# Performance work log

Measured on AMD Instinct MI355X. Metric: run time of the kernel, lower is better.

Reference implementation:

```python
import jax, jax.numpy as jnp
import numpy as np

N_NODES = 10000
N_EDGES = 320000
IN_DIM = 512
HID = 64
H0 = 8
OUT = 64
H1 = 1
NEG_SLOPE = 0.2


def gat_layer(h, src, dst, W, attn_l, attn_r, n_nodes, activation=None):
    # h: (N, F_in); W: (F_in, H*D); attn_l/attn_r: (H, D)
    H, D = attn_l.shape
    feat = (h @ W).reshape(n_nodes, H, D)            # (N, H, D)
    el = jnp.einsum('nhd,hd->nh', feat, attn_l)      # (N, H)
    er = jnp.einsum('nhd,hd->nh', feat, attn_r)      # (N, H)
    e = jax.nn.leaky_relu(el[src] + er[dst], NEG_SLOPE)  # (E, H)
    # edge softmax over incoming edges of each destination node
    m = jax.ops.segment_max(e, dst, num_segments=n_nodes)   # (N, H), -inf for isolated
    m = jnp.where(jnp.isfinite(m), m, 0.0)
    ex = jnp.exp(e - m[dst])                         # (E, H)
    s = jax.ops.segment_sum(ex, dst, num_segments=n_nodes)  # (N, H)
    alpha = ex / s[dst]                              # (E, H)
    # weighted aggregation: out[dst] += alpha * feat[src]
    out = jax.ops.segment_sum(alpha[:, :, None] * feat[src], dst,
                              num_segments=n_nodes)  # (N, H, D)
    if activation is not None:
        out = activation(out)
    return out


def setup_inputs() -> dict:
    key = jax.random.key(0)
    ks = jax.random.split(key, 9)
    h = jax.random.normal(ks[0], (N_NODES, IN_DIM), dtype=jnp.float32)
    src = jax.random.randint(ks[1], (N_EDGES,), 0, N_NODES, dtype=jnp.int32)
    dst = jax.random.randint(ks[2], (N_EDGES,), 0, N_NODES, dtype=jnp.int32)
    W1 = jax.random.normal(ks[3], (IN_DIM, H0 * HID), dtype=jnp.float32) / np.sqrt(IN_DIM)
    attn_l1 = jax.random.normal(ks[4], (H0, HID), dtype=jnp.float32) / np.sqrt(HID)
    attn_r1 = jax.random.normal(ks[5], (H0, HID), dtype=jnp.float32) / np.sqrt(HID)
    W2 = jax.random.normal(ks[6], (H0 * HID, H1 * OUT), dtype=jnp.float32) / np.sqrt(H0 * HID)
    attn_l2 = jax.random.normal(ks[7], (H1, OUT), dtype=jnp.float32) / np.sqrt(OUT)
    attn_r2 = jax.random.normal(ks[8], (H1, OUT), dtype=jnp.float32) / np.sqrt(OUT)
    return {"h": h, "src": src, "dst": dst, "W1": W1, "attn_l1": attn_l1,
            "attn_r1": attn_r1, "W2": W2, "attn_l2": attn_l2, "attn_r2": attn_r2}


def reference(h, src, dst, W1, attn_l1, attn_r1, W2, attn_l2, attn_r2):
    # layer 1: elu activation, concat heads (flatten)
    x = gat_layer(h, src, dst, W1, attn_l1, attn_r1, N_NODES, activation=jax.nn.elu)
    x = x.reshape(N_NODES, H0 * HID)
    # layer 2: no activation, mean over heads
    x = gat_layer(x, src, dst, W2, attn_l2, attn_r2, N_NODES, activation=None)
    return x.mean(axis=1)  # (N, OUT)
```

## Files before the change

### kernel.cpp

```cpp
#include <hip/hip_runtime.h>
#include <hip/hip_bf16.h>
#include <math.h>

typedef unsigned int u32;
typedef unsigned short ushort;

constexpr int N_NODES = 10000;
constexpr int N_EDGES = 320000;
constexpr float NEG_SLOPE = 0.2f;

typedef __attribute__((ext_vector_type(8))) short short8;
typedef __attribute__((ext_vector_type(4))) float f32x4;
typedef __attribute__((ext_vector_type(16))) float f32x16;

__device__ __forceinline__ float lrelu(float x) { return x > 0.f ? x : NEG_SLOPE * x; }
__device__ __forceinline__ float elu(float x)   { return x > 0.f ? x : (expf(x) - 1.f); }

__device__ __forceinline__ ushort f2bf(float x) {
    u32 b = __float_as_uint(x);
    b += 0x7FFFu + ((b >> 16) & 1u);
    return (ushort)(b >> 16);
}
__device__ __forceinline__ float bf2f(ushort u) {
    return __uint_as_float(((u32)u) << 16);
}

__device__ __forceinline__ void gload16(const void* g, void* l) {
    __builtin_amdgcn_global_load_lds(
        (__attribute__((address_space(1))) void*)g,
        (__attribute__((address_space(3))) void*)l, 16, 0, 0);
}

constexpr int NB_SPLIT = (N_NODES * 512 / 4) / 256;
constexpr int NB_T1    = 64;
constexpr int NB_T2    = 8;
constexpr int NB_WLR2  = 2;
constexpr int NB_ZERO  = (N_NODES + 255) / 256;

__global__ void prep_kernel(const float4* __restrict__ h4,
                            ushort* __restrict__ hhi, ushort* __restrict__ hlo,
                            const float* __restrict__ W1,
                            ushort* __restrict__ w1thi, ushort* __restrict__ w1tlo,
                            const float* __restrict__ W2,
                            ushort* __restrict__ w2thi, ushort* __restrict__ w2tlo,
                            const float* __restrict__ al2, const float* __restrict__ ar2,
                            float* __restrict__ wl2, float* __restrict__ wr2,
                            int* __restrict__ counts) {
    __shared__ float smem[64][65];
    const int b = blockIdx.x;
    if (b < NB_SPLIT) {
        const int i = b * 256 + threadIdx.x;
        const float4 v = h4[i];
        ushort h0 = f2bf(v.x), h1 = f2bf(v.y), h2 = f2bf(v.z), h3 = f2bf(v.w);
        *(ushort4*)&hhi[i * 4] = make_ushort4(h0, h1, h2, h3);
        *(ushort4*)&hlo[i * 4] = make_ushort4(
            f2bf(v.x - bf2f(h0)), f2bf(v.y - bf2f(h1)),
            f2bf(v.z - bf2f(h2)), f2bf(v.w - bf2f(h3)));
    } else if (b < NB_SPLIT + NB_T1 + NB_T2) {
        const bool isW1 = b < NB_SPLIT + NB_T1;
        const float* W = isW1 ? W1 : W2;
        ushort* thi = isW1 ? w1thi : w2thi;
        ushort* tlo = isW1 ? w1tlo : w2tlo;
        const int N  = isW1 ? 512 : 64;
        const int t  = isW1 ? (b - NB_SPLIT) : (b - NB_SPLIT - NB_T1);
        const int ti = isW1 ? (t & 7) : t;
        const int tj = isW1 ? (t >> 3) : 0;
        const int c  = threadIdx.x & 63;
        const int r0 = threadIdx.x >> 6;
#pragma unroll
        for (int p = 0; p < 16; p++) {
            const int r = p * 4 + r0;
            smem[r][c] = W[(size_t)(ti * 64 + r) * N + tj * 64 + c];
        }
        __syncthreads();
#pragma unroll
        for (int p = 0; p < 16; p++) {
            const int rr = p * 4 + r0;
            const float v = smem[c][rr];
            const ushort hh = f2bf(v);
            thi[(size_t)(tj * 64 + rr) * 512 + ti * 64 + c] = hh;
            tlo[(size_t)(tj * 64 + rr) * 512 + ti * 64 + c] = f2bf(v - bf2f(hh));
        }
    } else if (b < NB_SPLIT + NB_T1 + NB_T2 + NB_WLR2) {
        const int k = (b - NB_SPLIT - NB_T1 - NB_T2) * 256 + threadIdx.x;
        float sl = 0.f, sr = 0.f;
#pragma unroll 8
        for (int d = 0; d < 64; d++) {
            const float w = W2[(size_t)k * 64 + d];
            sl += w * al2[d];
            sr += w * ar2[d];
        }
        wl2[k] = sl;
        wr2[k] = sr;
    } else {
        const int j = (b - NB_SPLIT - NB_T1 - NB_T2 - NB_WLR2) * 256 + threadIdx.x;
        if (j < N_NODES) counts[j] = 0;
    }
}

__global__ __launch_bounds__(256) void gemm1_kernel(
    const ushort* __restrict__ Ahi, const ushort* __restrict__ Alo,
    const ushort* __restrict__ Bhi, const ushort* __restrict__ Blo,
    ushort* __restrict__ Cout, int M,
    const float* __restrict__ attn_l, const float* __restrict__ attn_r,
    float* __restrict__ elp, float* __restrict__ erp) {
    constexpr int BM = 64, BN = 128, BK = 32, K = 512, N = 512;

    __shared__ __align__(16) ushort sAhi[BM * BK];
    __shared__ __align__(16) ushort sAlo[BM * BK];
    __shared__ __align__(16) ushort sBhi[BN * BK];
    __shared__ __align__(16) ushort sBlo[BN * BK];

    const int tid = threadIdx.x;
    const int wave = tid >> 6, lane = tid & 63;
    const int m0 = blockIdx.x * BM, n0 = blockIdx.y * BN;
    const int wm = wave >> 1, wn = wave & 1;
    const int l31 = lane & 31, lh = lane >> 5;

    const int fb = wave * 1024 + lane * 16;

    int arow = m0 + (fb >> 6);
    if (arow > M - 1) arow = M - 1;
    const size_t abyte = (size_t)arow * (K * 2) + (fb & 63);
    size_t bbyte[2];
#pragma unroll
    for (int r = 0; r < 2; r++) {
        const int f = fb + r * 4096;
        bbyte[r] = (size_t)(n0 + (f >> 6)) * (K * 2) + (f & 63);
    }

    f32x16 acc[2] = {};

    for (int k0 = 0; k0 < K; k0 += BK) {
        __syncthreads();
        const size_t kb = (size_t)k0 * 2;
        gload16((const char*)Ahi + abyte + kb, (char*)sAhi + fb);
        gload16((const char*)Alo + abyte + kb, (char*)sAlo + fb);
#pragma unroll
        for (int r = 0; r < 2; r++) {
            const int f = fb + r * 4096;
            gload16((const char*)Bhi + bbyte[r] + kb, (char*)sBhi + f);
            gload16((const char*)Blo + bbyte[r] + kb, (char*)sBlo + f);
        }
        __syncthreads();

#pragma unroll
        for (int ks = 0; ks < 2; ks++) {
            const int koff = ks * 16 + lh * 8;
            const int arw = wm * 32 + l31;
            const short8 ah = *(const short8*)&sAhi[arw * BK + koff];
            const short8 al = *(const short8*)&sAlo[arw * BK + koff];
            short8 bh[2], bl[2];
#pragma unroll
            for (int ni = 0; ni < 2; ni++) {
                const int brw = wn * 64 + ni * 32 + l31;
                bh[ni] = *(const short8*)&sBhi[brw * BK + koff];
                bl[ni] = *(const short8*)&sBlo[brw * BK + koff];
            }
#pragma unroll
            for (int ni = 0; ni < 2; ni++) {
                acc[ni] = __builtin_amdgcn_mfma_f32_32x32x16_bf16(ah, bh[ni], acc[ni], 0, 0, 0);
                acc[ni] = __builtin_amdgcn_mfma_f32_32x32x16_bf16(ah, bl[ni], acc[ni], 0, 0, 0);
                acc[ni] = __builtin_amdgcn_mfma_f32_32x32x16_bf16(al, bh[ni], acc[ni], 0, 0, 0);
            }
        }
    }

#pragma unroll
    for (int reg = 0; reg < 16; reg++) {
        const int grow = m0 + wm * 32 + (reg & 3) + 8 * (reg >> 2) + 4 * lh;
        if (grow < M) {
#pragma unroll
            for (int ni = 0; ni < 2; ni++) {
                const int gcol = n0 + wn * 64 + ni * 32 + l31;
                Cout[(size_t)grow * N + gcol] = f2bf(acc[ni][reg]);
            }
        }
    }

    const int head = (n0 + wn * 64) >> 6;
    float alv[2], arv[2];
#pragma unroll
    for (int ni = 0; ni < 2; ni++) {
        alv[ni] = attn_l[head * 64 + ni * 32 + l31];
        arv[ni] = attn_r[head * 64 + ni * 32 + l31];
    }
#pragma unroll
    for (int reg = 0; reg < 16; reg++) {
        float pl = acc[0][reg] * alv[0] + acc[1][reg] * alv[1];
        float pr = acc[0][reg] * arv[0] + acc[1][reg] * arv[1];
#pragma unroll
        for (int o = 1; o < 32; o <<= 1) {
            pl += __shfl_xor(pl, o);
            pr += __shfl_xor(pr, o);
        }
        const int grow = m0 + wm * 32 + (reg & 3) + 8 * (reg >> 2) + 4 * lh;
        if (l31 == 0 && grow < M) {
            elp[grow * 8 + head] = pl;
            erp[grow * 8 + head] = pr;
        }
    }
}

__global__ __launch_bounds__(256) void gemm2_kernel(
    const ushort* __restrict__ Ahi, const ushort* __restrict__ Alo,
    const ushort* __restrict__ Bhi, const ushort* __restrict__ Blo,
    float* __restrict__ Cout, int M) {
    constexpr int BM = 64, BN = 64, BK = 32, K = 512, N = 64;
    constexpr int WM = 32, WN = 32, MT_M = 2, MT_N = 2;

    __shared__ __align__(16) ushort sAhi[BM * BK];
    __shared__ __align__(16) ushort sAlo[BM * BK];
    __shared__ __align__(16) ushort sBhi[BN * BK];
    __shared__ __align__(16) ushort sBlo[BN * BK];

    const int tid = threadIdx.x;
    const int wave = tid >> 6, lane = tid & 63;
    const int m0 = blockIdx.x * BM;
    const int wm = wave >> 1, wn = wave & 1;
    const int quad = lane >> 4, l15 = lane & 15;

    const int fb = wave * 1024 + lane * 16;

    int arow = m0 + (fb >> 6);
    if (arow > M - 1) arow = M - 1;
    const size_t abyte = (size_t)arow * (K * 2) + (fb & 63);
    const size_t bbyte = (size_t)(fb >> 6) * (K * 2) + (fb & 63);

    f32x4 acc[MT_M][MT_N] = {};

    for (int k0 = 0; k0 < K; k0 += BK) {
        __syncthreads();
        const size_t kb = (size_t)k0 * 2;
        gload16((const char*)Ahi + abyte + kb, (char*)sAhi + fb);
        gload16((const char*)Alo + abyte + kb, (char*)sAlo + fb);
        gload16((const char*)Bhi + bbyte + kb, (char*)sBhi + fb);
        gload16((const char*)Blo + bbyte + kb, (char*)sBlo + fb);
        __syncthreads();

        short8 ah[MT_M], al[MT_M], bh[MT_N], bl[MT_N];
#pragma unroll
        for (int mi = 0; mi < MT_M; mi++) {
            const int row = wm * WM + mi * 16 + l15;
            ah[mi] = *(const short8*)&sAhi[row * BK + quad * 8];
            al[mi] = *(const short8*)&sAlo[row * BK + quad * 8];
        }
#pragma unroll
        for (int ni = 0; ni < MT_N; ni++) {
            const int row = wn * WN + ni * 16 + l15;
            bh[ni] = *(const short8*)&sBhi[row * BK + quad * 8];
            bl[ni] = *(const short8*)&sBlo[row * BK + quad * 8];
        }
#pragma unroll
        for (int mi = 0; mi < MT_M; mi++)
#pragma unroll
            for (int ni = 0; ni < MT_N; ni++) {
                acc[mi][ni] = __builtin_amdgcn_mfma_f32_16x16x32_bf16(ah[mi], bh[ni], acc[mi][ni], 0, 0, 0);
                acc[mi][ni] = __builtin_amdgcn_mfma_f32_16x16x32_bf16(ah[mi], bl[ni], acc[mi][ni], 0, 0, 0);
                acc[mi][ni] = __builtin_amdgcn_mfma_f32_16x16x32_bf16(al[mi], bh[ni], acc[mi][ni], 0, 0, 0);
            }
    }

#pragma unroll
    for (int mi = 0; mi < MT_M; mi++) {
#pragma unroll
        for (int r = 0; r < 4; r++) {
            const int grow = m0 + wm * WM + mi * 16 + quad * 4 + r;
            if (grow < M) {
#pragma unroll
                for (int ni = 0; ni < MT_N; ni++) {
                    const int gcol = wn * WN + ni * 16 + l15;
                    Cout[(size_t)grow * N + gcol] = acc[mi][ni][r];
                }
            }
        }
    }
}

__global__ void hist_kernel(const int* __restrict__ dst, int* __restrict__ counts,
                            int* __restrict__ rank, int e) {
    const int i = blockIdx.x * 256 + threadIdx.x;
    if (i < e) rank[i] = atomicAdd(&counts[dst[i]], 1);
}

__global__ __launch_bounds__(1024) void scan_kernel(
    const int* __restrict__ counts, int* __restrict__ offs, int n) {
    __shared__ int wsum[16];
    const int tid = threadIdx.x;
    const int lane = tid & 63, wave = tid >> 6;
    const int base = tid * 10;
    int v[10];
    int s = 0;
#pragma unroll
    for (int i = 0; i < 10; i++) {
        v[i] = (base + i < n) ? counts[base + i] : 0;
        s += v[i];
    }
    int ps = s;
#pragma unroll
    for (int o = 1; o < 64; o <<= 1) {
        const int t = __shfl_up(ps, o);
        if (lane >= o) ps += t;
    }
    if (lane == 63) wsum[wave] = ps;
    __syncthreads();
    if (tid < 16) {
        int t = wsum[tid];
#pragma unroll
        for (int o = 1; o < 16; o <<= 1) {
            const int u = __shfl_up(t, o);
            if (tid >= o) t += u;
        }
        wsum[tid] = t;
    }
    __syncthreads();
    const int wbase = (wave > 0) ? wsum[wave - 1] : 0;
    int run = wbase + ps - s;
#pragma unroll
    for (int i = 0; i < 10; i++) {
        if (base + i < n) offs[base + i + 1] = run + v[i];
        run += v[i];
    }
    if (tid == 0) offs[0] = 0;
}

__global__ void scatter_kernel(const int* __restrict__ src, const int* __restrict__ dst,
                               const int* __restrict__ rank, const int* __restrict__ offs,
                               int* __restrict__ srcs, int e) {
    const int i = blockIdx.x * 256 + threadIdx.x;
    if (i < e) srcs[offs[dst[i]] + rank[i]] = src[i];
}

__global__ __launch_bounds__(256) void agg1_kernel(
    const ushort* __restrict__ feat, const float* __restrict__ el,
    const float* __restrict__ er, const int* __restrict__ offs,
    const int* __restrict__ srcs, ushort* __restrict__ xhi, ushort* __restrict__ xlo,
    const float* __restrict__ wl2, const float* __restrict__ wr2,
    float* __restrict__ el2, float* __restrict__ er2) {
    const int tid = threadIdx.x;
    const int wave = tid >> 6, lane = tid & 63;
    const int node = blockIdx.x * 4 + wave;
    const int start = offs[node];
    const int deg = offs[node + 1] - start;
    const int d0 = lane * 8;
    const int myh = lane >> 3;

    if (deg == 0) {
        const ushort4 z = make_ushort4(0, 0, 0, 0);
        *(ushort4*)&xhi[(size_t)node * 512 + d0] = z;
        *(ushort4*)&xhi[(size_t)node * 512 + d0 + 4] = z;
        *(ushort4*)&xlo[(size_t)node * 512 + d0] = z;
        *(ushort4*)&xlo[(size_t)node * 512 + d0 + 4] = z;
        if (lane == 0) { el2[node] = 0.f; er2[node] = 0.f; }
        return;
    }

    const float4 ea = *(const float4*)&er[node * 8];
    const float4 eb = *(const float4*)&er[node * 8 + 4];
    const float er_my = (myh & 4) ? ((myh & 2) ? ((myh & 1) ? eb.w : eb.z)
                                              : ((myh & 1) ? eb.y : eb.x))
                                  : ((myh & 2) ? ((myh & 1) ? ea.w : ea.z)
                                              : ((myh & 1) ? ea.y : ea.x));

    float acc[8];
#pragma unroll
    for (int i = 0; i < 8; i++) acc[i] = 0.f;
    float ws = 0.f;

    for (int base = 0; base < deg; base += 64) {
        const int has = min(64, deg - base);
        const int s = srcs[start + base + min(lane, has - 1)];
        int j = 0;
        for (; j + 8 <= has; j += 8) {
            int sq[8];
#pragma unroll
            for (int q = 0; q < 8; q++) sq[q] = __shfl(s, j + q);
            float eq[8];
#pragma unroll
            for (int q = 0; q < 8; q++) eq[q] = el[sq[q] * 8 + myh];
            short8 uq[8];
#pragma unroll
            for (int q = 0; q < 8; q++)
                uq[q] = *(const short8*)&feat[(size_t)sq[q] * 512 + d0];
            float wq[8];
#pragma unroll
            for (int q = 0; q < 8; q++) wq[q] = __expf(lrelu(eq[q] + er_my));
#pragma unroll
            for (int q = 0; q < 8; q++) {
#pragma unroll
                for (int i = 0; i < 8; i++)
                    acc[i] += wq[q] * bf2f((ushort)uq[q][i]);
                ws += wq[q];
            }
        }
        for (; j < has; j++) {
            const int sj = __shfl(s, j);
            const float w = __expf(lrelu(el[sj * 8 + myh] + er_my));
            const short8 u = *(const short8*)&feat[(size_t)sj * 512 + d0];
#pragma unroll
            for (int i = 0; i < 8; i++)
                acc[i] += w * bf2f((ushort)u[i]);
            ws += w;
        }
    }

    const float inv = 1.f / ws;
    float o[8];
#pragma unroll
    for (int i = 0; i < 8; i++) o[i] = elu(acc[i] * inv);

    const float4 wla = *(const float4*)&wl2[d0];
    const float4 wlb = *(const float4*)&wl2[d0 + 4];
    const float4 wra = *(const float4*)&wr2[d0];
    const float4 wrb = *(const float4*)&wr2[d0 + 4];
    float pl = o[0] * wla.x + o[1] * wla.y + o[2] * wla.z + o[3] * wla.w
             + o[4] * wlb.x + o[5] * wlb.y + o[6] * wlb.z + o[7] * wlb.w;
    float pr = o[0] * wra.x + o[1] * wra.y + o[2] * wra.z + o[3] * wra.w
             + o[4] * wrb.x + o[5] * wrb.y + o[6] * wrb.z + o[7] * wrb.w;
#pragma unroll
    for (int off = 32; off > 0; off >>= 1) {
        pl += __shfl_xor(pl, off);
        pr += __shfl_xor(pr, off);
    }
    if (lane == 0) { el2[node] = pl; er2[node] = pr; }

    ushort hi[8], lo[8];
#pragma unroll
    for (int i = 0; i < 8; i++) {
        hi[i] = f2bf(o[i]);
        lo[i] = f2bf(o[i] - bf2f(hi[i]));
    }
    *(ushort4*)&xhi[(size_t)node * 512 + d0]     = make_ushort4(hi[0], hi[1], hi[2], hi[3]);
    *(ushort4*)&xhi[(size_t)node * 512 + d0 + 4] = make_ushort4(hi[4], hi[5], hi[6], hi[7]);
    *(ushort4*)&xlo[(size_t)node * 512 + d0]     = make_ushort4(lo[0], lo[1], lo[2], lo[3]);
    *(ushort4*)&xlo[(size_t)node * 512 + d0 + 4] = make_ushort4(lo[4], lo[5], lo[6], lo[7]);
}

__global__ __launch_bounds__(256) void agg2_kernel(
    const float* __restrict__ feat, const float* __restrict__ el,
    const float* __restrict__ er, const int* __restrict__ offs,
    const int* __restrict__ srcs, float* __restrict__ out) {
    const int tid = threadIdx.x;
    const int wave = tid >> 6, lane = tid & 63;
    const int node = blockIdx.x * 4 + wave;
    const int start = offs[node];
    const int deg = offs[node + 1] - start;
    if (deg == 0) { out[(size_t)node * 64 + lane] = 0.f; return; }
    const float ern = er[node];

    float acc = 0.f, ws = 0.f;
    for (int base = 0; base < deg; base += 64) {
        const int has = min(64, deg - base);
        const int s = srcs[start + base + min(lane, has - 1)];
        const float w = __expf(lrelu(el[s] + ern));
        int j = 0;
        for (; j + 8 <= has; j += 8) {
            float aq[8]; int sq[8];
#pragma unroll
            for (int q = 0; q < 8; q++) { aq[q] = __shfl(w, j + q); sq[q] = __shfl(s, j + q); }
            float fq[8];
#pragma unroll
            for (int q = 0; q < 8; q++) fq[q] = feat[(size_t)sq[q] * 64 + lane];
#pragma unroll
            for (int q = 0; q < 8; q++) { acc += aq[q] * fq[q]; ws += aq[q]; }
        }
        for (; j < has; j++) {
            const float a = __shfl(w, j);
            const int sj = __shfl(s, j);
            acc += a * feat[(size_t)sj * 64 + lane];
            ws += a;
        }
    }
    out[(size_t)node * 64 + lane] = acc / ws;
}

extern "C" void kernel_launch(void* const* d_in, const int* in_sizes, int n_in,
                              void* d_out, int out_size, void* d_ws, size_t ws_size,
                              hipStream_t stream) {
    const float* h   = (const float*)d_in[0];
    const int*   src = (const int*)d_in[1];
    const int*   dst = (const int*)d_in[2];
    const float* W1  = (const float*)d_in[3];
    const float* al1 = (const float*)d_in[4];
    const float* ar1 = (const float*)d_in[5];
    const float* W2  = (const float*)d_in[6];
    const float* al2 = (const float*)d_in[7];
    const float* ar2 = (const float*)d_in[8];
    float* out = (float*)d_out;

    char* p = (char*)d_ws;
    ushort* feat1bf = (ushort*)p; p += (size_t)N_NODES * 512 * 2;
    float* feat2 = (float*)p;  p += (size_t)N_NODES * 64 * 4;
    float* el1   = (float*)p;  p += (size_t)N_NODES * 8 * 4;
    float* er1   = (float*)p;  p += (size_t)N_NODES * 8 * 4;
    float* el2   = (float*)p;  p += (size_t)N_NODES * 4;
    float* er2   = (float*)p;  p += (size_t)N_NODES * 4;
    ushort* xhi  = (ushort*)p; p += (size_t)N_NODES * 512 * 2;
    ushort* xlo  = (ushort*)p; p += (size_t)N_NODES * 512 * 2;
    ushort* w1thi = (ushort*)p; p += (size_t)512 * 512 * 2;
    ushort* w1tlo = (ushort*)p; p += (size_t)512 * 512 * 2;
    ushort* w2thi = (ushort*)p; p += (size_t)64 * 512 * 2;
    ushort* w2tlo = (ushort*)p; p += (size_t)64 * 512 * 2;
    float* wl2   = (float*)p;  p += (size_t)512 * 4;
    float* wr2   = (float*)p;  p += (size_t)512 * 4;
    int* counts  = (int*)p;    p += (size_t)N_NODES * 4;
    int* offs    = (int*)p;    p += (size_t)10004 * 4;
    int* rank    = (int*)p;    p += (size_t)N_EDGES * 4;
    int* srcs    = (int*)p;    p += (size_t)N_EDGES * 4;

    prep_kernel<<<NB_SPLIT + NB_T1 + NB_T2 + NB_WLR2 + NB_ZERO, 256, 0, stream>>>(
        (const float4*)h, xhi, xlo, W1, w1thi, w1tlo, W2, w2thi, w2tlo,
        al2, ar2, wl2, wr2, counts);

    hist_kernel<<<(N_EDGES + 255) / 256, 256, 0, stream>>>(dst, counts, rank, N_EDGES);
    scan_kernel<<<1, 1024, 0, stream>>>(counts, offs, N_NODES);
    scatter_kernel<<<(N_EDGES + 255) / 256, 256, 0, stream>>>(src, dst, rank, offs, srcs, N_EDGES);

    {
        dim3 grid((N_NODES + 63) / 64, 512 / 128);
        gemm1_kernel<<<grid, 256, 0, stream>>>(
            xhi, xlo, w1thi, w1tlo, feat1bf, N_NODES, al1, ar1, el1, er1);
    }
    agg1_kernel<<<N_NODES / 4, 256, 0, stream>>>(
        feat1bf, el1, er1, offs, srcs, xhi, xlo, wl2, wr2, el2, er2);

    gemm2_kernel<<<(N_NODES + 63) / 64, 256, 0, stream>>>(
        xhi, xlo, w2thi, w2tlo, feat2, N_NODES);
    agg2_kernel<<<N_NODES / 4, 256, 0, stream>>>(feat2, el2, er2, offs, srcs, out);
}
```

Before: 217.8 us.

## Merge histogram into prep kernel and scatter into gemm1 launch

The standalone histogram and CSR scatter kernels are removed. The histogram becomes extra blocks in the prep kernel, and the scatter becomes extra blocks in a combined gemm1 launch using a flattened 1D grid. Zeroing of counts and the layer-2 attention projection move into a new small zero kernel that runs first. This cuts the launch count and lets the independent, latency-bound edge work overlap with the h split and the GEMM, at the cost of one extra small launch and mixed-block kernels.

```diff
diff --git a/kernel.cpp b/kernel.cpp
--- a/kernel.cpp
+++ b/kernel.cpp
@@ -31,11 +31,33 @@
         (__attribute__((address_space(3))) void*)l, 16, 0, 0);
 }
 
+constexpr int NBZ_CNT = (N_NODES + 255) / 256;
+__global__ void zero_kernel(int* __restrict__ counts,
+                            const float* __restrict__ W2,
+                            const float* __restrict__ al2, const float* __restrict__ ar2,
+                            float* __restrict__ wl2, float* __restrict__ wr2) {
+    const int b = blockIdx.x;
+    if (b < NBZ_CNT) {
+        const int j = b * 256 + threadIdx.x;
+        if (j < N_NODES) counts[j] = 0;
+    } else {
+        const int k = (b - NBZ_CNT) * 256 + threadIdx.x;
+        float sl = 0.f, sr = 0.f;
+#pragma unroll 8
+        for (int d = 0; d < 64; d++) {
+            const float w = W2[(size_t)k * 64 + d];
+            sl += w * al2[d];
+            sr += w * ar2[d];
+        }
+        wl2[k] = sl;
+        wr2[k] = sr;
+    }
+}
+
 constexpr int NB_SPLIT = (N_NODES * 512 / 4) / 256;
 constexpr int NB_T1    = 64;
 constexpr int NB_T2    = 8;
-constexpr int NB_WLR2  = 2;
-constexpr int NB_ZERO  = (N_NODES + 255) / 256;
+constexpr int NB_HIST  = (N_EDGES + 255) / 256;
 
 __global__ void prep_kernel(const float4* __restrict__ h4,
                             ushort* __restrict__ hhi, ushort* __restrict__ hlo,
@@ -43,26 +65,28 @@
                             ushort* __restrict__ w1thi, ushort* __restrict__ w1tlo,
                             const float* __restrict__ W2,
                             ushort* __restrict__ w2thi, ushort* __restrict__ w2tlo,
-                            const float* __restrict__ al2, const float* __restrict__ ar2,
-                            float* __restrict__ wl2, float* __restrict__ wr2,
-                            int* __restrict__ counts) {
+                            const int* __restrict__ dst, int* __restrict__ counts,
+                            int* __restrict__ rank) {
     __shared__ float smem[64][65];
     const int b = blockIdx.x;
-    if (b < NB_SPLIT) {
+    if (b < NB_HIST) {
         const int i = b * 256 + threadIdx.x;
+        if (i < N_EDGES) rank[i] = atomicAdd(&counts[dst[i]], 1);
+    } else if (b < NB_HIST + NB_SPLIT) {
+        const int i = (b - NB_HIST) * 256 + threadIdx.x;
         const float4 v = h4[i];
         ushort h0 = f2bf(v.x), h1 = f2bf(v.y), h2 = f2bf(v.z), h3 = f2bf(v.w);
         *(ushort4*)&hhi[i * 4] = make_ushort4(h0, h1, h2, h3);
         *(ushort4*)&hlo[i * 4] = make_ushort4(
             f2bf(v.x - bf2f(h0)), f2bf(v.y - bf2f(h1)),
             f2bf(v.z - bf2f(h2)), f2bf(v.w - bf2f(h3)));
-    } else if (b < NB_SPLIT + NB_T1 + NB_T2) {
-        const bool isW1 = b < NB_SPLIT + NB_T1;
+    } else {
+        const bool isW1 = b < NB_HIST + NB_SPLIT + NB_T1;
         const float* W = isW1 ? W1 : W2;
         ushort* thi = isW1 ? w1thi : w2thi;
         ushort* tlo = isW1 ? w1tlo : w2tlo;
         const int N  = isW1 ? 512 : 64;
-        const int t  = isW1 ? (b - NB_SPLIT) : (b - NB_SPLIT - NB_T1);
+        const int t  = isW1 ? (b - NB_HIST - NB_SPLIT) : (b - NB_HIST - NB_SPLIT - NB_T1);
         const int ti = isW1 ? (t & 7) : t;
         const int tj = isW1 ? (t >> 3) : 0;
         const int c  = threadIdx.x & 63;
@@ -81,30 +105,69 @@
             thi[(size_t)(tj * 64 + rr) * 512 + ti * 64 + c] = hh;
             tlo[(size_t)(tj * 64 + rr) * 512 + ti * 64 + c] = f2bf(v - bf2f(hh));
         }
-    } else if (b < NB_SPLIT + NB_T1 + NB_T2 + NB_WLR2) {
-        const int k = (b - NB_SPLIT - NB_T1 - NB_T2) * 256 + threadIdx.x;
-        float sl = 0.f, sr = 0.f;
-#pragma unroll 8
-        for (int d = 0; d < 64; d++) {
-            const float w = W2[(size_t)k * 64 + d];
-            sl += w * al2[d];
-            sr += w * ar2[d];
-        }
-        wl2[k] = sl;
-        wr2[k] = sr;
-    } else {
-        const int j = (b - NB_SPLIT - NB_T1 - NB_T2 - NB_WLR2) * 256 + threadIdx.x;
-        if (j < N_NODES) counts[j] = 0;
-    }
-}
-
-__global__ __launch_bounds__(256) void gemm1_kernel(
+    }
+}
+
+__global__ __launch_bounds__(1024) void scan_kernel(
+    const int* __restrict__ counts, int* __restrict__ offs, int n) {
+    __shared__ int wsum[16];
+    const int tid = threadIdx.x;
+    const int lane = tid & 63, wave = tid >> 6;
+    const int base = tid * 10;
+    int v[10];
+    int s = 0;
+#pragma unroll
+    for (int i = 0; i < 10; i++) {
+        v[i] = (base + i < n) ? counts[base + i] : 0;
+        s += v[i];
+    }
+    int ps = s;
+#pragma unroll
+    for (int o = 1; o < 64; o <<= 1) {
+        const int t = __shfl_up(ps, o);
+        if (lane >= o) ps += t;
+    }
+    if (lane == 63) wsum[wave] = ps;
+    __syncthreads();
+    if (tid < 16) {
+        int t = wsum[tid];
+#pragma unroll
+        for (int o = 1; o < 16; o <<= 1) {
+            const int u = __shfl_up(t, o);
+            if (tid >= o) t += u;
+        }
+        wsum[tid] = t;
+    }
+    __syncthreads();
+    const int wbase = (wave > 0) ? wsum[wave - 1] : 0;
+    int run = wbase + ps - s;
+#pragma unroll
+    for (int i = 0; i < 10; i++) {
+        if (base + i < n) offs[base + i + 1] = run + v[i];
+        run += v[i];
+    }
+    if (tid == 0) offs[0] = 0;
+}
+
+constexpr int NB_GEMM1 = ((N_NODES + 63) / 64) * 4;
+constexpr int NB_SCAT  = (N_EDGES + 255) / 256;
+
+__global__ __launch_bounds__(256) void gemm1_scatter_kernel(
     const ushort* __restrict__ Ahi, const ushort* __restrict__ Alo,
     const ushort* __restrict__ Bhi, const ushort* __restrict__ Blo,
     ushort* __restrict__ Cout, int M,
     const float* __restrict__ attn_l, const float* __restrict__ attn_r,
-    float* __restrict__ elp, float* __restrict__ erp) {
+    float* __restrict__ elp, float* __restrict__ erp,
+    const int* __restrict__ src, const int* __restrict__ dst,
+    const int* __restrict__ rank, const int* __restrict__ offs,
+    int* __restrict__ srcs) {
     constexpr int BM = 64, BN = 128, BK = 32, K = 512, N = 512;
+
+    if ((int)blockIdx.x >= NB_GEMM1) {
+        const int i = ((int)blockIdx.x - NB_GEMM1) * 256 + threadIdx.x;
+        if (i < N_EDGES) srcs[offs[dst[i]] + rank[i]] = src[i];
+        return;
+    }
 
     __shared__ __align__(16) ushort sAhi[BM * BK];
     __shared__ __align__(16) ushort sAlo[BM * BK];
@@ -113,7 +176,7 @@
 
     const int tid = threadIdx.x;
     const int wave = tid >> 6, lane = tid & 63;
-    const int m0 = blockIdx.x * BM, n0 = blockIdx.y * BN;
+    const int m0 = ((int)blockIdx.x >> 2) * BM, n0 = ((int)blockIdx.x & 3) * BN;
     const int wm = wave >> 1, wn = wave & 1;
     const int l31 = lane & 31, lh = lane >> 5;
 
@@ -275,60 +338,6 @@
             }
         }
     }
-}
-
-__global__ void hist_kernel(const int* __restrict__ dst, int* __restrict__ counts,
-                            int* __restrict__ rank, int e) {
-    const int i = blockIdx.x * 256 + threadIdx.x;
-    if (i < e) rank[i] = atomicAdd(&counts[dst[i]], 1);
-}
-
-__global__ __launch_bounds__(1024) void scan_kernel(
-    const int* __restrict__ counts, int* __restrict__ offs, int n) {
-    __shared__ int wsum[16];
-    const int tid = threadIdx.x;
-    const int lane = tid & 63, wave = tid >> 6;
-    const int base = tid * 10;
-    int v[10];
-    int s = 0;
-#pragma unroll
-    for (int i = 0; i < 10; i++) {
-        v[i] = (base + i < n) ? counts[base + i] : 0;
-        s += v[i];
-    }
-    int ps = s;
-#pragma unroll
-    for (int o = 1; o < 64; o <<= 1) {
-        const int t = __shfl_up(ps, o);
-        if (lane >= o) ps += t;
-    }
-    if (lane == 63) wsum[wave] = ps;
-    __syncthreads();
-    if (tid < 16) {
-        int t = wsum[tid];
-#pragma unroll
-        for (int o = 1; o < 16; o <<= 1) {
-            const int u = __shfl_up(t, o);
-            if (tid >= o) t += u;
-        }
-        wsum[tid] = t;
-    }
-    __syncthreads();
-    const int wbase = (wave > 0) ? wsum[wave - 1] : 0;
-    int run = wbase + ps - s;
-#pragma unroll
-    for (int i = 0; i < 10; i++) {
-        if (base + i < n) offs[base + i + 1] = run + v[i];
-        run += v[i];
-    }
-    if (tid == 0) offs[0] = 0;
-}
-
-__global__ void scatter_kernel(const int* __restrict__ src, const int* __restrict__ dst,
-                               const int* __restrict__ rank, const int* __restrict__ offs,
-                               int* __restrict__ srcs, int e) {
-    const int i = blockIdx.x * 256 + threadIdx.x;
-    if (i < e) srcs[offs[dst[i]] + rank[i]] = src[i];
 }
 
 __global__ __launch_bounds__(256) void agg1_kernel(
@@ -508,23 +517,23 @@
     int* rank    = (int*)p;    p += (size_t)N_EDGES * 4;
     int* srcs    = (int*)p;    p += (size_t)N_EDGES * 4;
 
-    prep_kernel<<<NB_SPLIT + NB_T1 + NB_T2 + NB_WLR2 + NB_ZERO, 256, 0, stream>>>(
+    zero_kernel<<<NBZ_CNT + 2, 256, 0, stream>>>(counts, W2, al2, ar2, wl2, wr2);
+
+    prep_kernel<<<NB_HIST + NB_SPLIT + NB_T1 + NB_T2, 256, 0, stream>>>(
         (const float4*)h, xhi, xlo, W1, w1thi, w1tlo, W2, w2thi, w2tlo,
-        al2, ar2, wl2, wr2, counts);
-
-    hist_kernel<<<(N_EDGES + 255) / 256, 256, 0, stream>>>(dst, counts, rank, N_EDGES);
+        dst, counts, rank);
+
     scan_kernel<<<1, 1024, 0, stream>>>(counts, offs, N_NODES);
-    scatter_kernel<<<(N_EDGES + 255) / 256, 256, 0, stream>>>(src, dst, rank, offs, srcs, N_EDGES);
-
-    {
-        dim3 grid((N_NODES + 63) / 64, 512 / 128);
-        gemm1_kernel<<<grid, 256, 0, stream>>>(
-            xhi, xlo, w1thi, w1tlo, feat1bf, N_NODES, al1, ar1, el1, er1);
-    }
+
+    gemm1_scatter_kernel<<<NB_GEMM1 + NB_SCAT, 256, 0, stream>>>(
+        xhi, xlo, w1thi, w1tlo, feat1bf, N_NODES, al1, ar1, el1, er1,
+        src, dst, rank, offs, srcs);
+
     agg1_kernel<<<N_NODES / 4, 256, 0, stream>>>(
         feat1bf, el1, er1, offs, srcs, xhi, xlo, wl2, wr2, el2, er2);
 
     gemm2_kernel<<<(N_NODES + 63) / 64, 256, 0, stream>>>(
         xhi, xlo, w2thi, w2tlo, feat2, N_NODES);
+
     agg2_kernel<<<N_NODES / 4, 256, 0, stream>>>(feat2, el2, er2, offs, srcs, out);
 }
```

Result: faster. 213.5 us (-2.0%).
